# Performance work log

Measured on AMD Instinct MI355X. Metric: run time of the kernel, lower is better.

## Reference

```python
import jax, jax.numpy as jnp
import numpy as np

PW = 2        # positive_window
NM = 5        # negative_margin
TEMP = 0.1    # temperature
WEIGHT = 1.0
NEG_INF = -1e30


def setup_inputs() -> dict:
    key = jax.random.key(0)
    B, T, D = 64, 512, 1024
    hidden_states = jax.random.normal(key, (B, T, D), dtype=jnp.float32)
    return {"hidden_states": hidden_states}


def reference(hidden_states):
    B, T, D = hidden_states.shape
    # F.normalize(dim=-1): x / max(||x||, eps)
    norm = jnp.linalg.norm(hidden_states, axis=-1, keepdims=True)
    feats = hidden_states / jnp.maximum(norm, 1e-12)  # [B,T,D]

    # Only t with neg_start = t+NM < T-1 contribute a loss term.
    Tv = T - NM - 1                      # number of valid anchors
    t_idx = jnp.arange(Tv)               # [Tv]

    # positives: mean of feats at offsets {-PW..-1, 1..PW}, clipped to >=0
    offsets = jnp.concatenate([jnp.arange(-PW, 0), jnp.arange(1, PW + 1)])  # [2*PW]
    pos_idx = t_idx[:, None] + offsets[None, :]        # [Tv, 2*PW]
    pos_mask = (pos_idx >= 0) & (pos_idx < T)
    pos_idx_c = jnp.clip(pos_idx, 0, T - 1)
    pos_feats = feats[:, pos_idx_c]                    # [B, Tv, 2*PW, D]
    pos_cnt = pos_mask.sum(axis=1).astype(feats.dtype)  # [Tv]
    positives = (pos_feats * pos_mask[None, :, :, None].astype(feats.dtype)).sum(axis=2) \
                / pos_cnt[None, :, None]               # [B, Tv, D]

    anchors = feats[:, :Tv]                            # [B, Tv, D]
    pos_score = jnp.einsum('btd,btd->bt', anchors, positives) / TEMP   # [B, Tv]

    # negatives: feats[:, t+NM:] -> full scores masked where s < t+NM
    neg_scores = jnp.einsum('btd,bsd->bts', anchors, feats) / TEMP     # [B, Tv, T]
    s_idx = jnp.arange(T)
    neg_mask = s_idx[None, :] >= (t_idx[:, None] + NM)  # [Tv, T]
    neg_scores = jnp.where(neg_mask[None], neg_scores, NEG_INF)

    all_scores = jnp.concatenate([pos_score[:, :, None], neg_scores], axis=-1)  # [B, Tv, 1+T]
    # cross-entropy with label 0, averaged over batch per t, then over t
    loss_bt = jax.nn.logsumexp(all_scores, axis=-1) - pos_score  # [B, Tv]
    return loss_bt.mean() * WEIGHT
```

## Files before the change

kernel.cpp:

```cpp
#include <hip/hip_runtime.h>
#include <hip/hip_bf16.h>
#include <math.h>

constexpr int   Bc       = 64;
constexpr int   Tc       = 512;
constexpr int   Dc       = 1024;
constexpr int   NMc      = 5;
constexpr int   TvC      = Tc - NMc - 1;
constexpr float TEMP_INV = 10.0f;

using bf16x8 = __attribute__((ext_vector_type(8))) short;
using f32x4  = __attribute__((ext_vector_type(4))) float;

__device__ inline short f2bf(float f) {
    unsigned u = __float_as_uint(f);
    unsigned r = (u + 0x7fffu + ((u >> 16) & 1u)) >> 16;
    return (short)r;
}
__device__ inline float wave_reduce_sum(float v) {
#pragma unroll
    for (int off = 32; off; off >>= 1) v += __shfl_xor(v, off);
    return v;
}

#define GLOAD16(gp, lp)                                                        \
    __builtin_amdgcn_global_load_lds(                                          \
        (const __attribute__((address_space(1))) void*)(gp),                   \
        (__attribute__((address_space(3))) void*)(lp), 16, 0, 0)

__global__ __launch_bounds__(256) void tcl_prep(const float* __restrict__ h,
                                                short* __restrict__ fb,
                                                float* __restrict__ out) {
    if (blockIdx.x == 0 && threadIdx.x == 0) *out = 0.f;
    const int row  = blockIdx.x * 4 + (threadIdx.x >> 6);
    const int lane = threadIdx.x & 63;
    const float4* h4 = reinterpret_cast<const float4*>(h) + (size_t)row * 256 + lane;
    float4 v[4];
    float ss = 0.f;
#pragma unroll
    for (int i = 0; i < 4; ++i) {
        v[i] = h4[i * 64];
        ss += v[i].x*v[i].x + v[i].y*v[i].y + v[i].z*v[i].z + v[i].w*v[i].w;
    }
    ss = wave_reduce_sum(ss);
    const float inv = 1.0f / fmaxf(sqrtf(ss), 1e-12f);
    short4* o4 = reinterpret_cast<short4*>(fb + (size_t)row * Dc) + lane;
#pragma unroll
    for (int i = 0; i < 4; ++i) {
        short4 o;
        o.x = f2bf(v[i].x * inv); o.y = f2bf(v[i].y * inv);
        o.z = f2bf(v[i].z * inv); o.w = f2bf(v[i].w * inv);
        o4[i * 64] = o;
    }
}

__device__ __constant__ unsigned char JOB_TI[20] =
    {0,1, 0,1,2,3, 0,1,2,3,4,5, 0,1,2,3,4,5,6,7};
__device__ __constant__ unsigned char JOB_SJ[20] =
    {0,0, 1,1,1,1, 2,2,2,2,2,2, 3,3,3,3,3,3,3,3};

__global__ __launch_bounds__(256) void tcl_scores(const short* __restrict__ fb,
                                                  float* __restrict__ S_part,
                                                  float* __restrict__ pos_d,
                                                  float* __restrict__ pos_x) {
    const int p  = blockIdx.x;
    const int b  = (p & 7) * 8 + ((p >> 3) / 20);
    const int j  = (p >> 3) % 20;
    const int ti = (int)JOB_TI[j];
    const int sj = (int)JOB_SJ[j];
    const int t0 = ti * 64;
    const int s0 = sj * 128;
    const bool is_diag = (ti == 2 * sj) || (ti == 2 * sj + 1);
    const bool is_x    = (ti == 2 * sj - 1);

    const short* f = fb + (size_t)b * Tc * Dc;
    const int lane = threadIdx.x & 63;
    const int wid  = threadIdx.x >> 6;
    const int wr   = wid >> 1, wc = wid & 1;

    __shared__ short Als[64 * 64];
    __shared__ short Bls[128 * 64];

    const int sub = lane >> 3;
    const int c8  = lane & 7;
    const int csw = (c8 ^ sub) << 3;
    const short* gA[2]; const short* gB[4];
    short* lA[2]; short* lB[4];
#pragma unroll
    for (int i = 0; i < 2; ++i) {
        const int ri = wid * 2 + i;
        gA[i] = f + (size_t)(t0 + ri * 8 + sub) * Dc + csw;
        lA[i] = Als + ri * 512;
    }
#pragma unroll
    for (int i = 0; i < 4; ++i) {
        const int ri = wid * 4 + i;
        gB[i] = f + (size_t)(s0 + ri * 8 + sub) * Dc + csw;
        lB[i] = Bls + ri * 512;
    }

    const int r16 = lane & 15, kg = lane >> 4;
    int aoff[2][2], boff[4][2];
#pragma unroll
    for (int ks = 0; ks < 2; ++ks) {
        const int cb = (ks * 64 + kg * 16) ^ ((r16 & 7) << 4);
#pragma unroll
        for (int q = 0; q < 2; ++q)
            aoff[q][ks] = (wr * 32 + q * 16 + r16) * 64 + (cb >> 1);
#pragma unroll
        for (int q = 0; q < 4; ++q)
            boff[q][ks] = (wc * 64 + q * 16 + r16) * 64 + (cb >> 1);
    }

    f32x4 acc[2][4];
#pragma unroll
    for (int fa = 0; fa < 2; ++fa)
#pragma unroll
        for (int fbj = 0; fbj < 4; ++fbj) acc[fa][fbj] = f32x4{0.f, 0.f, 0.f, 0.f};

    for (int kt = 0; kt < 16; ++kt) {
#pragma unroll
        for (int i = 0; i < 2; ++i) { GLOAD16(gA[i], lA[i]); gA[i] += 64; }
#pragma unroll
        for (int i = 0; i < 4; ++i) { GLOAD16(gB[i], lB[i]); gB[i] += 64; }
        __syncthreads();

        bf16x8 av[2][2], bv[4][2];
#pragma unroll
        for (int ks = 0; ks < 2; ++ks) {
#pragma unroll
            for (int q = 0; q < 2; ++q) av[q][ks] = *(const bf16x8*)(Als + aoff[q][ks]);
#pragma unroll
            for (int q = 0; q < 4; ++q) bv[q][ks] = *(const bf16x8*)(Bls + boff[q][ks]);
        }
#pragma unroll
        for (int fa = 0; fa < 2; ++fa)
#pragma unroll
            for (int fbj = 0; fbj < 4; ++fbj)
#pragma unroll
                for (int ks = 0; ks < 2; ++ks)
                    acc[fa][fbj] = __builtin_amdgcn_mfma_f32_16x16x32_bf16(
                        av[fa][ks], bv[fbj][ks], acc[fa][fbj], 0, 0, 0);
        __syncthreads();
    }

    __shared__ float S_sh[2][64];
    __shared__ float P_sh[2][64];
#pragma unroll
    for (int fa = 0; fa < 2; ++fa) {
#pragma unroll
        for (int r = 0; r < 4; ++r) {
            const int trow = t0 + wr * 32 + fa * 16 + kg * 4 + r;
            float v = 0.f, pv = 0.f;
#pragma unroll
            for (int fbj = 0; fbj < 4; ++fbj) {
                const int col = s0 + wc * 64 + fbj * 16 + r16;
                const float sc = acc[fa][fbj][r] * TEMP_INV;
                v += (col >= trow + NMc) ? __expf(sc - 10.f) : 0.f;
                const int dd = col - trow;
                pv += (dd * dd == 1 || dd * dd == 4) ? sc : 0.f;
            }
#pragma unroll
            for (int off = 1; off < 16; off <<= 1) {
                v  += __shfl_xor(v, off);
                pv += __shfl_xor(pv, off);
            }
            if (r16 == 0) {
                const int rl = wr * 32 + fa * 16 + kg * 4 + r;
                S_sh[wc][rl] = v;
                P_sh[wc][rl] = pv;
            }
        }
    }

    if (is_x && wr == 1 && wc == 0) {
        float cv = 0.f;
        const int c = s0 + r16;
#pragma unroll
        for (int fa = 0; fa < 2; ++fa)
#pragma unroll
            for (int r = 0; r < 4; ++r) {
                const int trow = t0 + 32 + fa * 16 + kg * 4 + r;
                const int dd = c - trow;
                cv += (dd == 1 || dd == 2) ? acc[fa][0][r] * TEMP_INV : 0.f;
            }
        cv += __shfl_xor(cv, 16);
        cv += __shfl_xor(cv, 32);
        if (kg == 0 && r16 < 2) pos_x[(size_t)b * Tc + c] = cv;
    }

    __syncthreads();
    if (threadIdx.x < 64) {
        const int t = t0 + threadIdx.x;
        S_part[((size_t)b * 4 + sj) * Tc + t] = S_sh[0][threadIdx.x] + S_sh[1][threadIdx.x];
        const float pr = P_sh[0][threadIdx.x] + P_sh[1][threadIdx.x];
        if (is_diag)
            pos_d[(size_t)b * Tc + t] = pr;
        if (is_x && threadIdx.x >= 62)
            pos_x[(size_t)b * Tc + t] = pr;
    }
}

__global__ __launch_bounds__(256) void tcl_combine(const float* __restrict__ S_part,
                                                   const float* __restrict__ pos_d,
                                                   const float* __restrict__ pos_x,
                                                   float* __restrict__ out, float scale) {
    const int b = blockIdx.x;
    float lsum = 0.f;
    for (int t = threadIdx.x; t < TvC; t += 256) {
        const int ti = t >> 7, tl = t & 127;
        float S = 0.f;
        for (int sj = ti; sj < 4; ++sj) S += S_part[((size_t)b * 4 + sj) * Tc + t];
        float praw = pos_d[(size_t)b * Tc + t];
        if ((tl >= 126 && ti < 3) || (tl <= 1 && ti > 0))
            praw += pos_x[(size_t)b * Tc + t];
        const float cnt = (t == 0) ? 2.f : (t == 1) ? 3.f : 4.f;
        const float pos = praw / cnt;
        lsum += __logf(__expf(pos - 10.f) + S) + 10.f - pos;
    }
    lsum = wave_reduce_sum(lsum);
    __shared__ float wls[4];
    const int lane = threadIdx.x & 63, wid = threadIdx.x >> 6;
    if (lane == 0) wls[wid] = lsum;
    __syncthreads();
    if (threadIdx.x == 0)
        atomicAdd(out, (wls[0] + wls[1] + wls[2] + wls[3]) * scale);
}

extern "C" void kernel_launch(void* const* d_in, const int* in_sizes, int n_in,
                              void* d_out, int out_size, void* d_ws, size_t ws_size,
                              hipStream_t stream) {
    const float* h = (const float*)d_in[0];
    float* out = (float*)d_out;

    const size_t feats_bytes = (size_t)Bc * Tc * Dc * sizeof(short);
    const size_t spart_bytes = (size_t)Bc * 4 * Tc * sizeof(float);
    const size_t posd_bytes  = (size_t)Bc * Tc * sizeof(float);
    const float  scale       = 1.0f / (float)(Bc * TvC);

    short* fb     = (short*)d_ws;
    float* S_part = (float*)((char*)d_ws + feats_bytes);
    float* pos_d  = (float*)((char*)d_ws + feats_bytes + spart_bytes);
    float* pos_x  = (float*)((char*)d_ws + feats_bytes + spart_bytes + posd_bytes);

    tcl_prep<<<Bc * Tc / 4, 256, 0, stream>>>(h, fb, out);
    tcl_scores<<<Bc * 20, 256, 0, stream>>>(fb, S_part, pos_d, pos_x);
    tcl_combine<<<Bc, 256, 0, stream>>>(S_part, pos_d, pos_x, out, scale);
    (void)ws_size; (void)in_sizes; (void)n_in; (void)out_size;
}
```

Baseline: 69.96 us.

## Double-buffer LDS tiles to overlap global loads with MFMA compute

The GEMM main loop now uses two LDS buffers for the A and B tiles. It issues the next k-tile's global-to-LDS loads before computing on the current buffer, and the loop is unrolled by two to alternate buffers. The aim is to hide global memory latency behind MFMA work instead of loading and then stalling at each barrier. In exchange LDS use doubles, which may lower occupancy, and the correctness of the overlap depends on how GLOAD16 is synchronised.

Measured after the change: 75.62 us. 1.08x slower.

```diff
diff --git a/kernel.cpp b/kernel.cpp
--- a/kernel.cpp
+++ b/kernel.cpp
@@ -78,26 +78,40 @@
     const int wid  = threadIdx.x >> 6;
     const int wr   = wid >> 1, wc = wid & 1;
 
-    __shared__ short Als[64 * 64];
-    __shared__ short Bls[128 * 64];
+    __shared__ short Als[2 * 64 * 64];
+    __shared__ short Bls[2 * 128 * 64];
 
     const int sub = lane >> 3;
     const int c8  = lane & 7;
     const int csw = (c8 ^ sub) << 3;
     const short* gA[2]; const short* gB[4];
-    short* lA[2]; short* lB[4];
+    int lAo[2]; int lBo[4];
 #pragma unroll
     for (int i = 0; i < 2; ++i) {
         const int ri = wid * 2 + i;
         gA[i] = f + (size_t)(t0 + ri * 8 + sub) * Dc + csw;
-        lA[i] = Als + ri * 512;
+        lAo[i] = ri * 512;
     }
 #pragma unroll
     for (int i = 0; i < 4; ++i) {
         const int ri = wid * 4 + i;
         gB[i] = f + (size_t)(s0 + ri * 8 + sub) * Dc + csw;
-        lB[i] = Bls + ri * 512;
-    }
+        lBo[i] = ri * 512;
+    }
+
+#define STAGE(BUF)                                                             \
+    do {                                                                       \
+        _Pragma("unroll")                                                      \
+        for (int i = 0; i < 2; ++i) {                                          \
+            GLOAD16(gA[i], Als + (BUF) * 4096 + lAo[i]);                       \
+            gA[i] += 64;                                                       \
+        }                                                                      \
+        _Pragma("unroll")                                                      \
+        for (int i = 0; i < 4; ++i) {                                          \
+            GLOAD16(gB[i], Bls + (BUF) * 8192 + lBo[i]);                       \
+            gB[i] += 64;                                                       \
+        }                                                                      \
+    } while (0)
 
     const int r16 = lane & 15, kg = lane >> 4;
     int aoff[2][2], boff[4][2];
@@ -118,31 +132,40 @@
 #pragma unroll
         for (int fbj = 0; fbj < 4; ++fbj) acc[fa][fbj] = f32x4{0.f, 0.f, 0.f, 0.f};
 
-    for (int kt = 0; kt < 16; ++kt) {
-#pragma unroll
-        for (int i = 0; i < 2; ++i) { GLOAD16(gA[i], lA[i]); gA[i] += 64; }
-#pragma unroll
-        for (int i = 0; i < 4; ++i) { GLOAD16(gB[i], lB[i]); gB[i] += 64; }
+#define COMPUTE(BUF)                                                           \
+    do {                                                                       \
+        bf16x8 av[2][2], bv[4][2];                                             \
+        _Pragma("unroll")                                                      \
+        for (int ks = 0; ks < 2; ++ks) {                                       \
+            _Pragma("unroll")                                                  \
+            for (int q = 0; q < 2; ++q)                                        \
+                av[q][ks] = *(const bf16x8*)(Als + (BUF) * 4096 + aoff[q][ks]);\
+            _Pragma("unroll")                                                  \
+            for (int q = 0; q < 4; ++q)                                        \
+                bv[q][ks] = *(const bf16x8*)(Bls + (BUF) * 8192 + boff[q][ks]);\
+        }                                                                      \
+        _Pragma("unroll")                                                      \
+        for (int fa = 0; fa < 2; ++fa)                                         \
+            _Pragma("unroll")                                                  \
+            for (int fbj = 0; fbj < 4; ++fbj)                                  \
+                _Pragma("unroll")                                              \
+                for (int ks = 0; ks < 2; ++ks)                                 \
+                    acc[fa][fbj] = __builtin_amdgcn_mfma_f32_16x16x32_bf16(    \
+                        av[fa][ks], bv[fbj][ks], acc[fa][fbj], 0, 0, 0);       \
+    } while (0)
+
+    STAGE(0);
+    __syncthreads();
+    for (int kt = 0; kt < 16; kt += 2) {
+        STAGE(1);
+        COMPUTE(0);
         __syncthreads();
-
-        bf16x8 av[2][2], bv[4][2];
-#pragma unroll
-        for (int ks = 0; ks < 2; ++ks) {
-#pragma unroll
-            for (int q = 0; q < 2; ++q) av[q][ks] = *(const bf16x8*)(Als + aoff[q][ks]);
-#pragma unroll
-            for (int q = 0; q < 4; ++q) bv[q][ks] = *(const bf16x8*)(Bls + boff[q][ks]);
-        }
-#pragma unroll
-        for (int fa = 0; fa < 2; ++fa)
-#pragma unroll
-            for (int fbj = 0; fbj < 4; ++fbj)
-#pragma unroll
-                for (int ks = 0; ks < 2; ++ks)
-                    acc[fa][fbj] = __builtin_amdgcn_mfma_f32_16x16x32_bf16(
-                        av[fa][ks], bv[fbj][ks], acc[fa][fbj], 0, 0, 0);
+        if (kt < 14) STAGE(0);
+        COMPUTE(1);
         __syncthreads();
     }
+#undef STAGE
+#undef COMPUTE
 
     __shared__ float S_sh[2][64];
     __shared__ float P_sh[2][64];
```

## Quantize normalized features to FP8 e4m3 and use FP8 MFMA for scores

Applied to the files above, without the earlier changes.

Normalized features are now stored as FP8 e4m3 bytes with a software round-to-nearest-even encoder instead of bf16, halving the workspace write and the reads in the scoring GEMM. The score kernel switches to 16x16x32 fp8 MFMA with 128-byte K tiles, so it needs half as many K iterations, and the LDS swizzle is reworked for byte layout. The cost is a large precision loss on unit-norm features with D=1024, whose elements are tiny and fall into the subnormal range, so scores scaled by 10 may drift from the reference tolerance.

Measured after the change: 59.12 us. 1.18x faster.

```diff
diff --git a/kernel.cpp b/kernel.cpp
--- a/kernel.cpp
+++ b/kernel.cpp
@@ -9,18 +9,32 @@
 constexpr int   TvC      = Tc - NMc - 1;
 constexpr float TEMP_INV = 10.0f;
 
-using bf16x8 = __attribute__((ext_vector_type(8))) short;
-using f32x4  = __attribute__((ext_vector_type(4))) float;
-
-__device__ inline short f2bf(float f) {
-    unsigned u = __float_as_uint(f);
-    unsigned r = (u + 0x7fffu + ((u >> 16) & 1u)) >> 16;
-    return (short)r;
-}
+using f32x4 = __attribute__((ext_vector_type(4))) float;
+
 __device__ inline float wave_reduce_sum(float v) {
 #pragma unroll
     for (int off = 32; off; off >>= 1) v += __shfl_xor(v, off);
     return v;
+}
+
+__device__ inline unsigned char f2e4m3(float f) {
+    unsigned u = __float_as_uint(f);
+    unsigned s = (u >> 24) & 0x80u;
+    float a = __uint_as_float(u & 0x7fffffffu);
+    if (a >= 448.f) return (unsigned char)(s | 0x7Eu);
+    int Ef = (int)((u >> 23) & 0xFFu) - 127;
+    unsigned r;
+    if (Ef < -6) {
+        int n = (int)rintf(a * 512.0f);
+        r = (unsigned)n;
+    } else {
+        unsigned m23 = u & 0x7fffffu;
+        unsigned m = (m23 + 0x7ffffu + ((m23 >> 20) & 1u)) >> 20;
+        int E = Ef + 7;
+        if (m == 8u) { m = 0u; E += 1; }
+        r = ((unsigned)E << 3) | m;
+    }
+    return (unsigned char)(s | r);
 }
 
 #define GLOAD16(gp, lp)                                                        \
@@ -29,7 +43,7 @@
         (__attribute__((address_space(3))) void*)(lp), 16, 0, 0)
 
 __global__ __launch_bounds__(256) void tcl_prep(const float* __restrict__ h,
-                                                short* __restrict__ fb,
+                                                unsigned char* __restrict__ fq,
                                                 float* __restrict__ out) {
     if (blockIdx.x == 0 && threadIdx.x == 0) *out = 0.f;
     const int row  = blockIdx.x * 4 + (threadIdx.x >> 6);
@@ -44,13 +58,14 @@
     }
     ss = wave_reduce_sum(ss);
     const float inv = 1.0f / fmaxf(sqrtf(ss), 1e-12f);
-    short4* o4 = reinterpret_cast<short4*>(fb + (size_t)row * Dc) + lane;
+    unsigned* o4 = reinterpret_cast<unsigned*>(fq + (size_t)row * Dc);
 #pragma unroll
     for (int i = 0; i < 4; ++i) {
-        short4 o;
-        o.x = f2bf(v[i].x * inv); o.y = f2bf(v[i].y * inv);
-        o.z = f2bf(v[i].z * inv); o.w = f2bf(v[i].w * inv);
-        o4[i * 64] = o;
+        const unsigned pk = (unsigned)f2e4m3(v[i].x * inv)
+                          | ((unsigned)f2e4m3(v[i].y * inv) << 8)
+                          | ((unsigned)f2e4m3(v[i].z * inv) << 16)
+                          | ((unsigned)f2e4m3(v[i].w * inv) << 24);
+        o4[lane + i * 64] = pk;
     }
 }
 
@@ -59,7 +74,7 @@
 __device__ __constant__ unsigned char JOB_SJ[20] =
     {0,0, 1,1,1,1, 2,2,2,2,2,2, 3,3,3,3,3,3,3,3};
 
-__global__ __launch_bounds__(256) void tcl_scores(const short* __restrict__ fb,
+__global__ __launch_bounds__(256) void tcl_scores(const unsigned char* __restrict__ fq,
                                                   float* __restrict__ S_part,
                                                   float* __restrict__ pos_d,
                                                   float* __restrict__ pos_x) {
@@ -73,44 +88,39 @@
     const bool is_diag = (ti == 2 * sj) || (ti == 2 * sj + 1);
     const bool is_x    = (ti == 2 * sj - 1);
 
-    const short* f = fb + (size_t)b * Tc * Dc;
+    const unsigned char* f = fq + (size_t)b * Tc * Dc;
     const int lane = threadIdx.x & 63;
     const int wid  = threadIdx.x >> 6;
     const int wr   = wid >> 1, wc = wid & 1;
 
-    __shared__ short Als[64 * 64];
-    __shared__ short Bls[128 * 64];
+    __shared__ __align__(16) unsigned char Als[64 * 128];
+    __shared__ __align__(16) unsigned char Bls[128 * 128];
 
     const int sub = lane >> 3;
     const int c8  = lane & 7;
-    const int csw = (c8 ^ sub) << 3;
-    const short* gA[2]; const short* gB[4];
-    short* lA[2]; short* lB[4];
+    const int cswb = (c8 ^ sub) << 4;
+    const unsigned char* gA[2]; const unsigned char* gB[4];
+    int lAo[2]; int lBo[4];
 #pragma unroll
     for (int i = 0; i < 2; ++i) {
         const int ri = wid * 2 + i;
-        gA[i] = f + (size_t)(t0 + ri * 8 + sub) * Dc + csw;
-        lA[i] = Als + ri * 512;
+        gA[i] = f + (size_t)(t0 + ri * 8 + sub) * Dc + cswb;
+        lAo[i] = ri * 1024;
     }
 #pragma unroll
     for (int i = 0; i < 4; ++i) {
         const int ri = wid * 4 + i;
-        gB[i] = f + (size_t)(s0 + ri * 8 + sub) * Dc + csw;
-        lB[i] = Bls + ri * 512;
+        gB[i] = f + (size_t)(s0 + ri * 8 + sub) * Dc + cswb;
+        lBo[i] = ri * 1024;
     }
 
     const int r16 = lane & 15, kg = lane >> 4;
-    int aoff[2][2], boff[4][2];
-#pragma unroll
-    for (int ks = 0; ks < 2; ++ks) {
-        const int cb = (ks * 64 + kg * 16) ^ ((r16 & 7) << 4);
-#pragma unroll
-        for (int q = 0; q < 2; ++q)
-            aoff[q][ks] = (wr * 32 + q * 16 + r16) * 64 + (cb >> 1);
-#pragma unroll
-        for (int q = 0; q < 4; ++q)
-            boff[q][ks] = (wc * 64 + q * 16 + r16) * 64 + (cb >> 1);
-    }
+    const int kgh = kg >> 1, kgl = kg & 1;
+    int arow[2], brow[4];
+#pragma unroll
+    for (int q = 0; q < 2; ++q) arow[q] = (wr * 32 + q * 16 + r16) * 128;
+#pragma unroll
+    for (int q = 0; q < 4; ++q) brow[q] = (wc * 64 + q * 16 + r16) * 128;
 
     f32x4 acc[2][4];
 #pragma unroll
@@ -118,29 +128,31 @@
 #pragma unroll
         for (int fbj = 0; fbj < 4; ++fbj) acc[fa][fbj] = f32x4{0.f, 0.f, 0.f, 0.f};
 
-    for (int kt = 0; kt < 16; ++kt) {
-#pragma unroll
-        for (int i = 0; i < 2; ++i) { GLOAD16(gA[i], lA[i]); gA[i] += 64; }
-#pragma unroll
-        for (int i = 0; i < 4; ++i) { GLOAD16(gB[i], lB[i]); gB[i] += 64; }
+    for (int kt = 0; kt < 8; ++kt) {
+#pragma unroll
+        for (int i = 0; i < 2; ++i) { GLOAD16(gA[i], Als + lAo[i]); gA[i] += 128; }
+#pragma unroll
+        for (int i = 0; i < 4; ++i) { GLOAD16(gB[i], Bls + lBo[i]); gB[i] += 128; }
         __syncthreads();
 
-        bf16x8 av[2][2], bv[4][2];
-#pragma unroll
-        for (int ks = 0; ks < 2; ++ks) {
-#pragma unroll
-            for (int q = 0; q < 2; ++q) av[q][ks] = *(const bf16x8*)(Als + aoff[q][ks]);
-#pragma unroll
-            for (int q = 0; q < 4; ++q) bv[q][ks] = *(const bf16x8*)(Bls + boff[q][ks]);
+#pragma unroll
+        for (int ksub = 0; ksub < 4; ++ksub) {
+            const int g  = ksub * 2 + kgh;
+            const int bo = (((g ^ (r16 & 7)) << 4) | (kgl << 3));
+            long long av[2], bv[4];
+#pragma unroll
+            for (int q = 0; q < 2; ++q)
+                av[q] = *(const long long*)(Als + arow[q] + bo);
+#pragma unroll
+            for (int q = 0; q < 4; ++q)
+                bv[q] = *(const long long*)(Bls + brow[q] + bo);
+#pragma unroll
+            for (int fa = 0; fa < 2; ++fa)
+#pragma unroll
+                for (int fbj = 0; fbj < 4; ++fbj)
+                    acc[fa][fbj] = __builtin_amdgcn_mfma_f32_16x16x32_fp8_fp8(
+                        av[fa], bv[fbj], acc[fa][fbj], 0, 0, 0);
         }
-#pragma unroll
-        for (int fa = 0; fa < 2; ++fa)
-#pragma unroll
-            for (int fbj = 0; fbj < 4; ++fbj)
-#pragma unroll
-                for (int ks = 0; ks < 2; ++ks)
-                    acc[fa][fbj] = __builtin_amdgcn_mfma_f32_16x16x32_bf16(
-                        av[fa][ks], bv[fbj][ks], acc[fa][fbj], 0, 0, 0);
         __syncthreads();
     }
 
@@ -233,18 +245,18 @@
     const float* h = (const float*)d_in[0];
     float* out = (float*)d_out;
 
-    const size_t feats_bytes = (size_t)Bc * Tc * Dc * sizeof(short);
+    const size_t feats_bytes = (size_t)Bc * Tc * Dc;
     const size_t spart_bytes = (size_t)Bc * 4 * Tc * sizeof(float);
     const size_t posd_bytes  = (size_t)Bc * Tc * sizeof(float);
     const float  scale       = 1.0f / (float)(Bc * TvC);
 
-    short* fb     = (short*)d_ws;
+    unsigned char* fq = (unsigned char*)d_ws;
     float* S_part = (float*)((char*)d_ws + feats_bytes);
     float* pos_d  = (float*)((char*)d_ws + feats_bytes + spart_bytes);
     float* pos_x  = (float*)((char*)d_ws + feats_bytes + spart_bytes + posd_bytes);
 
-    tcl_prep<<<Bc * Tc / 4, 256, 0, stream>>>(h, fb, out);
-    tcl_scores<<<Bc * 20, 256, 0, stream>>>(fb, S_part, pos_d, pos_x);
+    tcl_prep<<<Bc * Tc / 4, 256, 0, stream>>>(h, fq, out);
+    tcl_scores<<<Bc * 20, 256, 0, stream>>>(fq, S_part, pos_d, pos_x);
     tcl_combine<<<Bc, 256, 0, stream>>>(S_part, pos_d, pos_x, out, scale);
     (void)ws_size; (void)in_sizes; (void)n_in; (void)out_size;
 }
```
